# Kernel optimization log

Hardware: AMD Instinct MI355X
Metric: run time of the kernel (lower is better)

The kernel has to match this reference:

```python
import jax, jax.numpy as jnp
import numpy as np

WS = 7   # window_size
SS = 3   # shift_size
NH = 4   # num_heads
EPS = 1e-5


def _ln(x, w, b):
    m = jnp.mean(x, axis=-1, keepdims=True)
    v = jnp.mean((x - m) ** 2, axis=-1, keepdims=True)
    return (x - m) / jnp.sqrt(v + EPS) * w + b


def _rel_index(ws):
    # relative position index [N, N], matches torch buffer construction
    coords = np.stack(np.meshgrid(np.arange(ws), np.arange(ws), indexing='ij'))  # [2,ws,ws]
    flat = coords.reshape(2, -1)                                                  # [2,N]
    rel = (flat[:, :, None] - flat[:, None, :]).transpose(1, 2, 0)                # [N,N,2]
    rel = rel + (ws - 1)
    return rel[..., 0] * (2 * ws - 1) + rel[..., 1]                               # [N,N]


def _shift_mask(H, W):
    # Faithful to source compute_mask, INCLUDING its unsqueeze(1)-unsqueeze(0)
    # construction which yields [nW, nW, N] (requires nW == N to broadcast).
    img = np.zeros((H, W), np.float32)
    cnt = 0
    for hs in (slice(0, -WS), slice(-WS, -SS), slice(-SS, None)):
        for wsl in (slice(0, -WS), slice(-WS, -SS), slice(-SS, None)):
            img[hs, wsl] = cnt
            cnt += 1
    mw = img.reshape(H // WS, WS, W // WS, WS).transpose(0, 2, 1, 3).reshape(-1, WS * WS)  # [nW,N]
    am = mw[:, None, :] - mw[None, :, :]                                                    # [nW,nW,N]
    am = np.where(am != 0, -100.0, 0.0).astype(np.float32)
    return jnp.asarray(am)


def setup_inputs() -> dict:
    key = jax.random.key(0)
    ks = jax.random.split(key, 8)
    B, H, W, C = 48, 49, 49, 128
    hid = 4 * C
    return {
        'x': jax.random.normal(ks[0], (B, H * W, C), jnp.float32),
        'norm1_w': jnp.ones((C,), jnp.float32),
        'norm1_b': jnp.zeros((C,), jnp.float32),
        'qkv_w': jax.random.normal(ks[1], (3 * C, C), jnp.float32) * 0.02,
        'qkv_b': jnp.zeros((3 * C,), jnp.float32),
        'proj_w': jax.random.normal(ks[2], (C, C), jnp.float32) * 0.02,
        'proj_b': jnp.zeros((C,), jnp.float32),
        'rpb_table': jax.random.normal(ks[3], ((2 * WS - 1) ** 2, NH), jnp.float32) * 0.02,
        'norm2_w': jnp.ones((C,), jnp.float32),
        'norm2_b': jnp.zeros((C,), jnp.float32),
        'fc1_w': jax.random.normal(ks[4], (hid, C), jnp.float32) * 0.02,
        'fc1_b': jnp.zeros((hid,), jnp.float32),
        'fc2_w': jax.random.normal(ks[5], (C, hid), jnp.float32) * 0.02,
        'fc2_b': jnp.zeros((C,), jnp.float32),
        'H': H,
        'W': W,
    }


def reference(x, norm1_w, norm1_b, qkv_w, qkv_b, proj_w, proj_b, rpb_table,
              norm2_w, norm2_b, fc1_w, fc1_b, fc2_w, fc2_b, H, W):
    B, L, C = x.shape
    hd = C // NH
    scale = hd ** -0.5
    nHw, nWw = H // WS, W // WS
    nW, N = nHw * nWw, WS * WS

    shortcut = x
    h = _ln(x, norm1_w, norm1_b).reshape(B, H, W, C)
    h = jnp.roll(h, (-SS, -SS), axis=(1, 2))  # cyclic shift

    # window partition -> [B*nW, N, C]
    xw = h.reshape(B, nHw, WS, nWw, WS, C).transpose(0, 1, 3, 2, 4, 5).reshape(B * nW, N, C)

    qkv = (xw @ qkv_w.T + qkv_b).reshape(B * nW, N, 3, NH, hd).transpose(2, 0, 3, 1, 4)
    q, k, v = qkv[0] * scale, qkv[1], qkv[2]  # [B*nW, NH, N, hd]

    attn = jnp.einsum('bhnd,bhmd->bhnm', q, k)  # [B*nW, NH, N, N]
    idx = _rel_index(WS)
    bias = rpb_table[idx.reshape(-1)].reshape(N, N, NH).transpose(2, 0, 1)  # [NH,N,N]
    attn = attn + bias[None]

    am = _shift_mask(H, W)  # [nW, nW, N]; broadcast exactly as source (nW == N)
    attn = attn.reshape(B, nW, NH, N, N) + am[None, :, None, :, :]
    attn = jax.nn.softmax(attn.reshape(B * nW, NH, N, N), axis=-1)

    out = jnp.einsum('bhnm,bhmd->bhnd', attn, v).transpose(0, 2, 1, 3).reshape(B * nW, N, C)
    out = out @ proj_w.T + proj_b

    # window reverse + reverse shift
    out = out.reshape(B, nHw, nWw, WS, WS, C).transpose(0, 1, 3, 2, 4, 5).reshape(B, H, W, C)
    out = jnp.roll(out, (SS, SS), axis=(1, 2)).reshape(B, H * W, C)

    x2 = shortcut + out
    m = _ln(x2, norm2_w, norm2_b)
    m = jax.nn.gelu(m @ fc1_w.T + fc1_b, approximate=False)
    return x2 + (m @ fc2_w.T + fc2_b)
```

## Files before the change

kernel.cpp:

```cpp
#include <hip/hip_runtime.h>
#include <math.h>

#define DEVFN __device__ __forceinline__

using short8 = __attribute__((ext_vector_type(8))) short;
using f32x4  = __attribute__((ext_vector_type(4))) float;

constexpr int Bc  = 48;
constexpr int HH  = 49;
constexpr int CC  = 128;
constexpr int NHd = 4;
constexpr int HD  = 32;
constexpr int SSz = 3;
constexpr int nWd = 49;
constexpr int NT  = 49;
constexpr int LL  = HH*HH;
constexpr int MR  = Bc*nWd*NT;

DEVFN unsigned short f2bf(float f){
  unsigned int u = __float_as_uint(f);
  u += 0x7fff + ((u >> 16) & 1);
  return (unsigned short)(u >> 16);
}
DEVFN float bf2f(unsigned short h){ return __uint_as_float(((unsigned)h) << 16); }

DEVFN int win_row_to_token(int r){
  int b   = r / (nWd*NT);
  int rem = r - b*(nWd*NT);
  int win = rem / NT;
  int t   = rem - win*NT;
  int hs  = (win/7)*7 + t/7;
  int ws_ = (win%7)*7 + t%7;
  int h = hs + SSz; if (h >= HH) h -= HH;
  int w = ws_ + SSz; if (w >= HH) w -= HH;
  return b*LL + h*HH + w;
}

DEVFN int rgn(int win, int tok){
  int hh = (win/7)*7 + tok/7;
  int ww = (win%7)*7 + tok%7;
  int rh = hh < 42 ? 0 : (hh < 46 ? 1 : 2);
  int rw = ww < 42 ? 0 : (ww < 46 ? 1 : 2);
  return rh*3 + rw;
}

__global__ __launch_bounds__(256) void ln1_gather(const float* __restrict__ x,
                                                  const float* __restrict__ w,
                                                  const float* __restrict__ b,
                                                  unsigned short* __restrict__ xw){
  int row  = blockIdx.x*4 + (threadIdx.x >> 6);
  int lane = threadIdx.x & 63;
  if (row >= MR) return;
  int token = win_row_to_token(row);
  float2 v = *(const float2*)(x + (size_t)token*CC + lane*2);
  float s  = v.x + v.y;
  float s2 = v.x*v.x + v.y*v.y;
  #pragma unroll
  for (int off = 32; off; off >>= 1){ s += __shfl_xor(s, off); s2 += __shfl_xor(s2, off); }
  float mean = s * (1.f/CC);
  float var  = s2 * (1.f/CC) - mean*mean;
  float rstd = rsqrtf(var + 1e-5f);
  ushort2 o;
  o.x = f2bf((v.x - mean)*rstd*w[lane*2+0] + b[lane*2+0]);
  o.y = f2bf((v.y - mean)*rstd*w[lane*2+1] + b[lane*2+1]);
  *(ushort2*)(xw + (size_t)row*CC + lane*2) = o;
}

__global__ __launch_bounds__(256) void ln2norm(const float* __restrict__ x2,
                                               const float* __restrict__ w,
                                               const float* __restrict__ b,
                                               unsigned short* __restrict__ xn){
  int row  = blockIdx.x*4 + (threadIdx.x >> 6);
  int lane = threadIdx.x & 63;
  if (row >= MR) return;
  float2 v = *(const float2*)(x2 + (size_t)row*CC + lane*2);
  float s  = v.x + v.y;
  float s2 = v.x*v.x + v.y*v.y;
  #pragma unroll
  for (int off = 32; off; off >>= 1){ s += __shfl_xor(s, off); s2 += __shfl_xor(s2, off); }
  float mean = s * (1.f/CC);
  float var  = s2 * (1.f/CC) - mean*mean;
  float rstd = rsqrtf(var + 1e-5f);
  ushort2 o;
  o.x = f2bf((v.x - mean)*rstd*w[lane*2+0] + b[lane*2+0]);
  o.y = f2bf((v.y - mean)*rstd*w[lane*2+1] + b[lane*2+1]);
  *(ushort2*)(xn + (size_t)row*CC + lane*2) = o;
}

__global__ __launch_bounds__(256) void attn_kernel(const unsigned short* __restrict__ qkv,
                                                   const float* __restrict__ rpb,
                                                   unsigned short* __restrict__ attno){
  __shared__ float k_s[NHd][NT*HD];
  __shared__ float v_s[NHd][NT*HD];
  __shared__ float rpb_s[169*NHd];
  int win  = blockIdx.x;
  int h    = threadIdx.x >> 6;
  int lane = threadIdx.x & 63;

  for (int i = threadIdx.x; i < 169*NHd; i += 256) rpb_s[i] = rpb[i];

  const unsigned short* base = qkv + (size_t)win*NT*384;
  for (int c = lane; c < NT*4; c += 64){
    int j = c >> 2, q8 = (c & 3)*8;
    short8 kv = *(const short8*)(base + j*384 + 128 + h*HD + q8);
    short8 vv = *(const short8*)(base + j*384 + 256 + h*HD + q8);
    #pragma unroll
    for (int e = 0; e < 8; ++e){
      k_s[h][j*HD + q8 + e] = bf2f((unsigned short)kv[e]);
      v_s[h][j*HD + q8 + e] = bf2f((unsigned short)vv[e]);
    }
  }
  __syncthreads();

  int i = lane;
  if (i >= NT) return;

  float q[HD];
  #pragma unroll
  for (int c = 0; c < 4; ++c){
    short8 qv = *(const short8*)(base + i*384 + h*HD + c*8);
    #pragma unroll
    for (int e = 0; e < 8; ++e) q[c*8+e] = bf2f((unsigned short)qv[e]) * 0.17677669529663689f;
  }

  int wmod = win % nWd;
  int yi = i/7, xi = i%7;

  float s[NT];
  #pragma unroll
  for (int j = 0; j < NT; ++j){
    float dot = 0.f;
    #pragma unroll
    for (int d4 = 0; d4 < HD/4; ++d4){
      float4 kv = *(const float4*)&k_s[h][j*HD + d4*4];
      dot = fmaf(q[d4*4+0], kv.x, dot);
      dot = fmaf(q[d4*4+1], kv.y, dot);
      dot = fmaf(q[d4*4+2], kv.z, dot);
      dot = fmaf(q[d4*4+3], kv.w, dot);
    }
    int yj = j/7, xj = j%7;
    int idx = (yi - yj + 6)*13 + (xi - xj + 6);
    float bias = rpb_s[idx*NHd + h];
    float mask = (rgn(wmod, j) != rgn(i, j)) ? -100.f : 0.f;
    s[j] = dot + bias + mask;
  }

  float m = -1e30f;
  #pragma unroll
  for (int j = 0; j < NT; ++j) m = fmaxf(m, s[j]);
  float sum = 0.f;
  #pragma unroll
  for (int j = 0; j < NT; ++j){ s[j] = __expf(s[j]-m); sum += s[j]; }
  float inv = 1.f/sum;

  float o[HD];
  #pragma unroll
  for (int d = 0; d < HD; ++d) o[d] = 0.f;
  #pragma unroll
  for (int j = 0; j < NT; ++j){
    float p = s[j]*inv;
    #pragma unroll
    for (int d4 = 0; d4 < HD/4; ++d4){
      float4 vv = *(const float4*)&v_s[h][j*HD + d4*4];
      o[d4*4+0] = fmaf(p, vv.x, o[d4*4+0]);
      o[d4*4+1] = fmaf(p, vv.y, o[d4*4+1]);
      o[d4*4+2] = fmaf(p, vv.z, o[d4*4+2]);
      o[d4*4+3] = fmaf(p, vv.w, o[d4*4+3]);
    }
  }

  unsigned short* op = attno + ((size_t)win*NT + i)*CC + h*HD;
  #pragma unroll
  for (int d4 = 0; d4 < HD/4; ++d4){
    ushort4 pk;
    pk.x = f2bf(o[d4*4+0]); pk.y = f2bf(o[d4*4+1]);
    pk.z = f2bf(o[d4*4+2]); pk.w = f2bf(o[d4*4+3]);
    *(ushort4*)(op + d4*4) = pk;
  }
}

template<int MODE, int Ntot, int KK>
__global__ __launch_bounds__(256) void gemm_bf16(const unsigned short* __restrict__ A,
                                                 const float* __restrict__ Wm,
                                                 const float* __restrict__ bias,
                                                 void* __restrict__ OutV,
                                                 const float* __restrict__ X){
  constexpr int BM = 128, BN = 128, BK = 64, LDK = 72;
  __shared__ unsigned short As[BM*LDK];
  __shared__ unsigned short Ws[BN*LDK];
  int tid  = threadIdx.x;
  int lane = tid & 63, wid = tid >> 6;
  int wr = wid >> 1, wc = wid & 1;
  int row0 = blockIdx.x*BM, col0 = blockIdx.y*BN;

  f32x4 acc[4][4] = {};

  for (int k0 = 0; k0 < KK; k0 += BK){
    #pragma unroll
    for (int p = 0; p < 4; ++p){
      int idx = p*256 + tid;
      int r = idx >> 3, c8 = (idx & 7)*8;
      int gr = row0 + r;
      short8 v = {};
      if (gr < MR) v = *(const short8*)(A + (size_t)gr*KK + k0 + c8);
      *(short8*)(As + r*LDK + c8) = v;
    }
    #pragma unroll
    for (int p = 0; p < 8; ++p){
      int idx = p*256 + tid;
      int r = idx >> 4, c4 = (idx & 15)*4;
      float4 wv = *(const float4*)(Wm + (size_t)(col0 + r)*KK + k0 + c4);
      ushort4 pk;
      pk.x = f2bf(wv.x); pk.y = f2bf(wv.y); pk.z = f2bf(wv.z); pk.w = f2bf(wv.w);
      *(ushort4*)(Ws + r*LDK + c4) = pk;
    }
    __syncthreads();

    int fr = lane & 15, fq = lane >> 4;
    #pragma unroll
    for (int kk = 0; kk < 2; ++kk){
      short8 a[4], b[4];
      #pragma unroll
      for (int m = 0; m < 4; ++m)
        a[m] = *(const short8*)(As + (wr*64 + m*16 + fr)*LDK + kk*32 + fq*8);
      #pragma unroll
      for (int n = 0; n < 4; ++n)
        b[n] = *(const short8*)(Ws + (wc*64 + n*16 + fr)*LDK + kk*32 + fq*8);
      #pragma unroll
      for (int m = 0; m < 4; ++m)
        #pragma unroll
        for (int n = 0; n < 4; ++n)
          acc[m][n] = __builtin_amdgcn_mfma_f32_16x16x32_bf16(a[m], b[n], acc[m][n], 0, 0, 0);
    }
    __syncthreads();
  }

  int fr = lane & 15, fq = lane >> 4;
  #pragma unroll
  for (int m = 0; m < 4; ++m){
    #pragma unroll
    for (int r = 0; r < 4; ++r){
      int grow = row0 + wr*64 + m*16 + fq*4 + r;
      if (grow >= MR) continue;
      int tok = 0;
      if constexpr (MODE == 1) tok = win_row_to_token(grow);
      #pragma unroll
      for (int n = 0; n < 4; ++n){
        int gcol = col0 + wc*64 + n*16 + fr;
        float v = acc[m][n][r] + bias[gcol];
        if constexpr (MODE == 0){
          ((unsigned short*)OutV)[(size_t)grow*Ntot + gcol] = f2bf(v);
        } else if constexpr (MODE == 1){
          ((float*)OutV)[(size_t)tok*CC + gcol] = v + X[(size_t)tok*CC + gcol];
        } else if constexpr (MODE == 2){
          v = 0.5f*v*(1.f + erff(v*0.70710678118654752f));
          ((unsigned short*)OutV)[(size_t)grow*Ntot + gcol] = f2bf(v);
        } else {
          float* p = (float*)OutV + (size_t)grow*CC + gcol;
          *p = *p + v;
        }
      }
    }
  }
}

extern "C" void kernel_launch(void* const* d_in, const int* in_sizes, int n_in,
                              void* d_out, int out_size, void* d_ws, size_t ws_size,
                              hipStream_t stream){
  const float* x      = (const float*)d_in[0];
  const float* n1w    = (const float*)d_in[1];
  const float* n1b    = (const float*)d_in[2];
  const float* qkv_w  = (const float*)d_in[3];
  const float* qkv_b  = (const float*)d_in[4];
  const float* proj_w = (const float*)d_in[5];
  const float* proj_b = (const float*)d_in[6];
  const float* rpb    = (const float*)d_in[7];
  const float* n2w    = (const float*)d_in[8];
  const float* n2b    = (const float*)d_in[9];
  const float* fc1_w  = (const float*)d_in[10];
  const float* fc1_b  = (const float*)d_in[11];
  const float* fc2_w  = (const float*)d_in[12];
  const float* fc2_b  = (const float*)d_in[13];
  float* out = (float*)d_out;

  char* ws = (char*)d_ws;
  const size_t U2 = (size_t)MR*CC*2;
  unsigned short* xw    = (unsigned short*)(ws);
  unsigned short* qkvb  = (unsigned short*)(ws + U2);
  unsigned short* attno = (unsigned short*)(ws);
  unsigned short* xn    = (unsigned short*)(ws + U2);
  unsigned short* hid   = (unsigned short*)(ws + 4*U2);

  const int lnBlocks = (MR + 3)/4;
  const int mBlocks  = (MR + 127)/128;

  ln1_gather<<<lnBlocks, 256, 0, stream>>>(x, n1w, n1b, xw);
  gemm_bf16<0,384,128><<<dim3(mBlocks,3), 256, 0, stream>>>(xw, qkv_w, qkv_b, qkvb, nullptr);
  attn_kernel<<<Bc*nWd, 256, 0, stream>>>(qkvb, rpb, attno);
  gemm_bf16<1,128,128><<<dim3(mBlocks,1), 256, 0, stream>>>(attno, proj_w, proj_b, out, x);
  ln2norm<<<lnBlocks, 256, 0, stream>>>(out, n2w, n2b, xn);
  gemm_bf16<2,512,128><<<dim3(mBlocks,4), 256, 0, stream>>>(xn, fc1_w, fc1_b, hid, nullptr);
  gemm_bf16<3,128,512><<<dim3(mBlocks,1), 256, 0, stream>>>(hid, fc2_w, fc2_b, out, nullptr);
}
```

Measured before the change: 577.4 us.

## Pre-convert weights to bf16 and restructure GEMMs around resident A tiles

Adds a small kernel that converts all weight matrices to bf16 once per call, so the GEMMs no longer convert fp32 weights inside every tile. The K=128 GEMMs now load a 256-row A tile into swizzled LDS once through direct global-to-LDS loads, keep it in registers, and loop over all output columns while reading B fragments straight from global/L2. FC2 gets its own kernel with a 256x128 output tile and K streamed in chunks. This cuts redundant A reloads and weight conversion across column blocks, at the cost of higher register pressure, uncached B reads from global memory and one extra launch.

```diff
diff --git a/kernel.cpp b/kernel.cpp
--- a/kernel.cpp
+++ b/kernel.cpp
@@ -24,6 +24,12 @@
 }
 DEVFN float bf2f(unsigned short h){ return __uint_as_float(((unsigned)h) << 16); }
 
+DEVFN void gload16(const unsigned short* g, unsigned short* l){
+  __builtin_amdgcn_global_load_lds((const __attribute__((address_space(1))) unsigned int*)g,
+                                   (__attribute__((address_space(3))) unsigned int*)l,
+                                   16, 0, 0);
+}
+
 DEVFN int win_row_to_token(int r){
   int b   = r / (nWd*NT);
   int rem = r - b*(nWd*NT);
@@ -42,6 +48,26 @@
   int rh = hh < 42 ? 0 : (hh < 46 ? 1 : 2);
   int rw = ww < 42 ? 0 : (ww < 46 ? 1 : 2);
   return rh*3 + rw;
+}
+
+__global__ __launch_bounds__(256) void wconv(const float* __restrict__ qkv_w,
+                                             const float* __restrict__ proj_w,
+                                             const float* __restrict__ fc1_w,
+                                             const float* __restrict__ fc2_w,
+                                             unsigned short* __restrict__ wq,
+                                             unsigned short* __restrict__ wp,
+                                             unsigned short* __restrict__ w1,
+                                             unsigned short* __restrict__ w2){
+  int b = blockIdx.x, t = threadIdx.x;
+  const float* src; unsigned short* dst; int base;
+  if (b < 48)      { src = qkv_w;  dst = wq; base = b*1024; }
+  else if (b < 64) { src = proj_w; dst = wp; base = (b-48)*1024; }
+  else if (b < 128){ src = fc1_w;  dst = w1; base = (b-64)*1024; }
+  else             { src = fc2_w;  dst = w2; base = (b-128)*1024; }
+  int i = base + t*4;
+  float4 v = *(const float4*)(src + i);
+  ushort4 o; o.x=f2bf(v.x); o.y=f2bf(v.y); o.z=f2bf(v.z); o.w=f2bf(v.w);
+  *(ushort4*)(dst + i) = o;
 }
 
 __global__ __launch_bounds__(256) void ln1_gather(const float* __restrict__ x,
@@ -179,86 +205,159 @@
   }
 }
 
-template<int MODE, int Ntot, int KK>
-__global__ __launch_bounds__(256) void gemm_bf16(const unsigned short* __restrict__ A,
-                                                 const float* __restrict__ Wm,
-                                                 const float* __restrict__ bias,
-                                                 void* __restrict__ OutV,
-                                                 const float* __restrict__ X){
-  constexpr int BM = 128, BN = 128, BK = 64, LDK = 72;
-  __shared__ unsigned short As[BM*LDK];
-  __shared__ unsigned short Ws[BN*LDK];
-  int tid  = threadIdx.x;
-  int lane = tid & 63, wid = tid >> 6;
-  int wr = wid >> 1, wc = wid & 1;
-  int row0 = blockIdx.x*BM, col0 = blockIdx.y*BN;
-
-  f32x4 acc[4][4] = {};
-
-  for (int k0 = 0; k0 < KK; k0 += BK){
-    #pragma unroll
-    for (int p = 0; p < 4; ++p){
-      int idx = p*256 + tid;
-      int r = idx >> 3, c8 = (idx & 7)*8;
-      int gr = row0 + r;
-      short8 v = {};
-      if (gr < MR) v = *(const short8*)(A + (size_t)gr*KK + k0 + c8);
-      *(short8*)(As + r*LDK + c8) = v;
-    }
-    #pragma unroll
-    for (int p = 0; p < 8; ++p){
-      int idx = p*256 + tid;
-      int r = idx >> 4, c4 = (idx & 15)*4;
-      float4 wv = *(const float4*)(Wm + (size_t)(col0 + r)*KK + k0 + c4);
-      ushort4 pk;
-      pk.x = f2bf(wv.x); pk.y = f2bf(wv.y); pk.z = f2bf(wv.z); pk.w = f2bf(wv.w);
-      *(ushort4*)(Ws + r*LDK + c4) = pk;
-    }
-    __syncthreads();
-
-    int fr = lane & 15, fq = lane >> 4;
-    #pragma unroll
-    for (int kk = 0; kk < 2; ++kk){
-      short8 a[4], b[4];
-      #pragma unroll
-      for (int m = 0; m < 4; ++m)
-        a[m] = *(const short8*)(As + (wr*64 + m*16 + fr)*LDK + kk*32 + fq*8);
-      #pragma unroll
-      for (int n = 0; n < 4; ++n)
-        b[n] = *(const short8*)(Ws + (wc*64 + n*16 + fr)*LDK + kk*32 + fq*8);
+template<int MODE, int NTOT>
+__global__ __launch_bounds__(256, 2) void gemm_k128(const unsigned short* __restrict__ A,
+                                                    const unsigned short* __restrict__ Wb,
+                                                    const float* __restrict__ bias,
+                                                    void* __restrict__ OutV,
+                                                    const float* __restrict__ X){
+  __shared__ __align__(16) unsigned short As[256*128];
+  int tid = threadIdx.x, lane = tid & 63, w = tid >> 6;
+  int fr = lane & 15, fq = lane >> 4;
+  int row0 = blockIdx.x * 256;
+
+  {
+    const unsigned short* Ab = A + (size_t)row0*128;
+    #pragma unroll
+    for (int i = 0; i < 16; ++i){
+      int L   = w*1024 + i*64 + lane;
+      int row = L >> 4;
+      int cg  = (L & 15) ^ (row & 15);
+      gload16(Ab + row*128 + cg*8, As + w*8192 + i*512);
+    }
+  }
+  __syncthreads();
+
+  short8 a[4][4];
+  #pragma unroll
+  for (int m = 0; m < 4; ++m)
+    #pragma unroll
+    for (int kc = 0; kc < 4; ++kc){
+      int row = w*64 + m*16 + fr;
+      int cs  = (kc*4 + fq) ^ fr;
+      a[m][kc] = *(const short8*)(As + row*128 + cs*8);
+    }
+
+  int tok_[4][4];
+  if constexpr (MODE == 1){
+    #pragma unroll
+    for (int m = 0; m < 4; ++m)
+      #pragma unroll
+      for (int r = 0; r < 4; ++r){
+        int grow = row0 + w*64 + m*16 + fq*4 + r;
+        tok_[m][r] = (grow < MR) ? win_row_to_token(grow) : 0;
+      }
+  }
+
+  for (int c0 = 0; c0 < NTOT; c0 += 64){
+    short8 b[4][4];
+    #pragma unroll
+    for (int n = 0; n < 4; ++n)
+      #pragma unroll
+      for (int kc = 0; kc < 4; ++kc)
+        b[n][kc] = *(const short8*)(Wb + (size_t)(c0 + n*16 + fr)*128 + kc*32 + fq*8);
+
+    f32x4 acc[4][4] = {};
+    #pragma unroll
+    for (int kc = 0; kc < 4; ++kc)
       #pragma unroll
       for (int m = 0; m < 4; ++m)
         #pragma unroll
         for (int n = 0; n < 4; ++n)
-          acc[m][n] = __builtin_amdgcn_mfma_f32_16x16x32_bf16(a[m], b[n], acc[m][n], 0, 0, 0);
+          acc[m][n] = __builtin_amdgcn_mfma_f32_16x16x32_bf16(a[m][kc], b[n][kc], acc[m][n], 0, 0, 0);
+
+    float bv[4];
+    #pragma unroll
+    for (int n = 0; n < 4; ++n) bv[n] = bias[c0 + n*16 + fr];
+
+    #pragma unroll
+    for (int m = 0; m < 4; ++m){
+      #pragma unroll
+      for (int r = 0; r < 4; ++r){
+        int grow = row0 + w*64 + m*16 + fq*4 + r;
+        if (grow >= MR) continue;
+        #pragma unroll
+        for (int n = 0; n < 4; ++n){
+          int gcol = c0 + n*16 + fr;
+          float v = acc[m][n][r] + bv[n];
+          if constexpr (MODE == 0){
+            ((unsigned short*)OutV)[(size_t)grow*NTOT + gcol] = f2bf(v);
+          } else if constexpr (MODE == 1){
+            int tok = tok_[m][r];
+            ((float*)OutV)[(size_t)tok*CC + gcol] = v + X[(size_t)tok*CC + gcol];
+          } else {
+            v = 0.5f*v*(1.f + erff(v*0.70710678118654752f));
+            ((unsigned short*)OutV)[(size_t)grow*NTOT + gcol] = f2bf(v);
+          }
+        }
+      }
+    }
+  }
+}
+
+__global__ __launch_bounds__(256, 2) void gemm_fc2(const unsigned short* __restrict__ A,
+                                                   const unsigned short* __restrict__ Wb,
+                                                   const float* __restrict__ bias,
+                                                   float* __restrict__ Out){
+  __shared__ __align__(16) unsigned short As[256*128];
+  int tid = threadIdx.x, lane = tid & 63, w = tid >> 6;
+  int fr = lane & 15, fq = lane >> 4;
+  int row0 = blockIdx.x * 256;
+
+  f32x4 acc[4][8] = {};
+
+  for (int kc0 = 0; kc0 < 4; ++kc0){
+    if (kc0) __syncthreads();
+    const unsigned short* Ab = A + (size_t)row0*512 + kc0*128;
+    #pragma unroll
+    for (int i = 0; i < 16; ++i){
+      int L   = w*1024 + i*64 + lane;
+      int row = L >> 4;
+      int cg  = (L & 15) ^ (row & 15);
+      gload16(Ab + (size_t)row*512 + cg*8, As + w*8192 + i*512);
     }
     __syncthreads();
-  }
-
-  int fr = lane & 15, fq = lane >> 4;
+
+    #pragma unroll
+    for (int kk = 0; kk < 2; ++kk){
+      short8 a[4][2];
+      #pragma unroll
+      for (int m = 0; m < 4; ++m)
+        #pragma unroll
+        for (int k2 = 0; k2 < 2; ++k2){
+          int row = w*64 + m*16 + fr;
+          int cs  = (kk*8 + k2*4 + fq) ^ fr;
+          a[m][k2] = *(const short8*)(As + row*128 + cs*8);
+        }
+      short8 b[8][2];
+      #pragma unroll
+      for (int n = 0; n < 8; ++n)
+        #pragma unroll
+        for (int k2 = 0; k2 < 2; ++k2)
+          b[n][k2] = *(const short8*)(Wb + (size_t)(n*16 + fr)*512 + kc0*128 + kk*64 + k2*32 + fq*8);
+      #pragma unroll
+      for (int k2 = 0; k2 < 2; ++k2)
+        #pragma unroll
+        for (int m = 0; m < 4; ++m)
+          #pragma unroll
+          for (int n = 0; n < 8; ++n)
+            acc[m][n] = __builtin_amdgcn_mfma_f32_16x16x32_bf16(a[m][k2], b[n][k2], acc[m][n], 0, 0, 0);
+    }
+  }
+
+  float bv[8];
+  #pragma unroll
+  for (int n = 0; n < 8; ++n) bv[n] = bias[n*16 + fr];
   #pragma unroll
   for (int m = 0; m < 4; ++m){
     #pragma unroll
     for (int r = 0; r < 4; ++r){
-      int grow = row0 + wr*64 + m*16 + fq*4 + r;
+      int grow = row0 + w*64 + m*16 + fq*4 + r;
       if (grow >= MR) continue;
-      int tok = 0;
-      if constexpr (MODE == 1) tok = win_row_to_token(grow);
-      #pragma unroll
-      for (int n = 0; n < 4; ++n){
-        int gcol = col0 + wc*64 + n*16 + fr;
-        float v = acc[m][n][r] + bias[gcol];
-        if constexpr (MODE == 0){
-          ((unsigned short*)OutV)[(size_t)grow*Ntot + gcol] = f2bf(v);
-        } else if constexpr (MODE == 1){
-          ((float*)OutV)[(size_t)tok*CC + gcol] = v + X[(size_t)tok*CC + gcol];
-        } else if constexpr (MODE == 2){
-          v = 0.5f*v*(1.f + erff(v*0.70710678118654752f));
-          ((unsigned short*)OutV)[(size_t)grow*Ntot + gcol] = f2bf(v);
-        } else {
-          float* p = (float*)OutV + (size_t)grow*CC + gcol;
-          *p = *p + v;
-        }
+      #pragma unroll
+      for (int n = 0; n < 8; ++n){
+        float* p = Out + (size_t)grow*CC + n*16 + fr;
+        *p = *p + acc[m][n][r] + bv[n];
       }
     }
   }
@@ -290,15 +389,20 @@
   unsigned short* attno = (unsigned short*)(ws);
   unsigned short* xn    = (unsigned short*)(ws + U2);
   unsigned short* hid   = (unsigned short*)(ws + 4*U2);
+  unsigned short* wq    = (unsigned short*)(ws + 8*U2);
+  unsigned short* wp    = wq + 49152;
+  unsigned short* w1    = wp + 16384;
+  unsigned short* w2    = w1 + 65536;
 
   const int lnBlocks = (MR + 3)/4;
-  const int mBlocks  = (MR + 127)/128;
-
+  const int mB256    = (MR + 255)/256;
+
+  wconv<<<192, 256, 0, stream>>>(qkv_w, proj_w, fc1_w, fc2_w, wq, wp, w1, w2);
   ln1_gather<<<lnBlocks, 256, 0, stream>>>(x, n1w, n1b, xw);
-  gemm_bf16<0,384,128><<<dim3(mBlocks,3), 256, 0, stream>>>(xw, qkv_w, qkv_b, qkvb, nullptr);
+  gemm_k128<0,384><<<mB256, 256, 0, stream>>>(xw, wq, qkv_b, qkvb, nullptr);
   attn_kernel<<<Bc*nWd, 256, 0, stream>>>(qkvb, rpb, attno);
-  gemm_bf16<1,128,128><<<dim3(mBlocks,1), 256, 0, stream>>>(attno, proj_w, proj_b, out, x);
+  gemm_k128<1,128><<<mB256, 256, 0, stream>>>(attno, wp, proj_b, out, x);
   ln2norm<<<lnBlocks, 256, 0, stream>>>(out, n2w, n2b, xn);
-  gemm_bf16<2,512,128><<<dim3(mBlocks,4), 256, 0, stream>>>(xn, fc1_w, fc1_b, hid, nullptr);
-  gemm_bf16<3,128,512><<<dim3(mBlocks,1), 256, 0, stream>>>(hid, fc2_w, fc2_b, out, nullptr);
-}
+  gemm_k128<2,512><<<mB256, 256, 0, stream>>>(xn, w1, fc1_b, hid, nullptr);
+  gemm_fc2<<<mB256, 256, 0, stream>>>(hid, w2, fc2_b, out);
+}
```

Measured after the change: 471.6 us. -18.3%, faster.
